# Optimization experiments

Measured on AMD Instinct MI355X. Metric: run time of the kernel, lower is better.

Reference implementation:

```python
import jax, jax.numpy as jnp
import numpy as np

B, S, D, N, R = 4, 2048, 1024, 64, 128

def setup_inputs() -> dict:
    key = jax.random.key(0)
    k1, k2, k3, k4, k5 = jax.random.split(key, 5)
    x = jax.random.normal(k1, (B, S, D), dtype=jnp.float32)
    feature_know_w = jax.random.uniform(k2, (B, S, N), dtype=jnp.float32)
    restore_know_w = jax.random.uniform(k3, (B, S, N), dtype=jnp.float32)
    # neuron pools, scaled like typical init
    feature_know = jax.random.normal(k4, (N, D, R), dtype=jnp.float32) / np.sqrt(D)
    restore_know = jax.random.normal(k5, (N, R, D), dtype=jnp.float32) / np.sqrt(R)
    return {"x": x, "feature_know_w": feature_know_w, "restore_know_w": restore_know_w,
            "feature_know": feature_know, "restore_know": restore_know}

def reference(x, feature_know_w, restore_know_w, feature_know, restore_know):
    # Feature stage: all_h[b,s,n,r] = sum_d x[b,s,d] * feature_know[n,d,r];
    # h[b,s,r] = sum_n all_h[b,s,n,r] * feature_know_w[b,s,n].
    # Fused into one einsum (same math, XLA picks pairwise contraction;
    # largest intermediate is [B,S,N,R], never [B,S,N,D]).
    h = jnp.einsum('bsd,ndr,bsn->bsr', x, feature_know, feature_know_w)
    # Restore stage: all_out[b,s,n,d] = sum_r h[b,s,r] * restore_know[n,r,d];
    # out[b,s,d] = sum_n all_out[b,s,n,d] * restore_know_w[b,s,n].
    # Reordered contraction keeps the intermediate at [B,S,N,R] instead of [B,S,N,D].
    out = jnp.einsum('bsr,bsn,nrd->bsd', h, restore_know_w, restore_know)
    # dropout p=0.0 -> identity
    return out
```

## Files before the change

kernel.cpp:

```cpp
#include <hip/hip_runtime.h>
#include <stdint.h>


typedef unsigned short ushort_t;
typedef __attribute__((ext_vector_type(8))) short frag_t;
typedef __attribute__((ext_vector_type(4))) float f32x4;

#define BK 64

__device__ __forceinline__ unsigned short f2bf(float f) {
    unsigned int u = __builtin_bit_cast(unsigned int, f);
    u = (u + 0x7FFFu + ((u >> 16) & 1u)) >> 16;
    return (unsigned short)u;
}
__device__ __forceinline__ float bf2f_lo(unsigned int v) {
    return __builtin_bit_cast(float, v << 16);
}
__device__ __forceinline__ float bf2f_hi(unsigned int v) {
    return __builtin_bit_cast(float, v & 0xFFFF0000u);
}

__device__ __forceinline__ void glds16(const ushort_t* g, ushort_t* l) {
    __builtin_amdgcn_global_load_lds(
        (const __attribute__((address_space(1))) unsigned int*)g,
        (__attribute__((address_space(3))) unsigned int*)l,
        16, 0, 0);
}

__global__ __launch_bounds__(256) void convert_bf(const float* __restrict__ in,
                                                  ushort_t* __restrict__ out, int n8) {
    int idx = blockIdx.x * 256 + threadIdx.x;
    if (idx >= n8) return;
    const float4 v0 = ((const float4*)in)[idx * 2];
    const float4 v1 = ((const float4*)in)[idx * 2 + 1];
    unsigned short b[8] = { f2bf(v0.x), f2bf(v0.y), f2bf(v0.z), f2bf(v0.w),
                            f2bf(v1.x), f2bf(v1.y), f2bf(v1.z), f2bf(v1.w) };
    ((uint4*)out)[idx] = *(const uint4*)b;
}

__global__ __launch_bounds__(256) void transpose_bf(const float* __restrict__ in,
                                                    ushort_t* __restrict__ out,
                                                    int R, int C,
                                                    long in_bstride, long out_bstride) {
    __shared__ float tile[64][65];
    in  += (long)blockIdx.z * in_bstride;
    out += (long)blockIdx.z * out_bstride;
    const int t  = threadIdx.x;
    const int r0 = blockIdx.x * 64;
    const int c0 = blockIdx.y * 64;
    const int ci = t & 63;
    const int rb = t >> 6;
    #pragma unroll
    for (int p = 0; p < 16; ++p)
        tile[rb + 4 * p][ci] = in[(size_t)(r0 + rb + 4 * p) * C + c0 + ci];
    __syncthreads();
    const int cw = t >> 2;
    const int rg = (t & 3) * 16;
    unsigned short buf[16];
    #pragma unroll
    for (int k = 0; k < 16; ++k)
        buf[k] = f2bf(tile[rg + k][cw]);
    uint4* dst = (uint4*)&out[(size_t)(c0 + cw) * R + r0 + rg];
    dst[0] = *(const uint4*)&buf[0];
    dst[1] = *(const uint4*)&buf[8];
}

__global__ __launch_bounds__(256) void mid_fuse(ushort_t* __restrict__ y,
                                                const float* __restrict__ w1,
                                                const float* __restrict__ w2) {
    const int m    = blockIdx.x * 4 + (threadIdx.x >> 6);
    const int lane = threadIdx.x & 63;
    unsigned int* yrow = (unsigned int*)(y + (size_t)m * 8192);
    const float* w1r = w1 + (size_t)m * 64;
    const float* w2r = w2 + (size_t)m * 64;
    float h0 = 0.f, h1 = 0.f;
    #pragma unroll 16
    for (int n = 0; n < 64; ++n) {
        const unsigned int v = yrow[n * 64 + lane];
        const float w = w1r[n];
        h0 += w * bf2f_lo(v);
        h1 += w * bf2f_hi(v);
    }
    #pragma unroll 16
    for (int n = 0; n < 64; ++n) {
        const float w = w2r[n];
        yrow[n * 64 + lane] =
            (unsigned int)f2bf(w * h0) | ((unsigned int)f2bf(w * h1) << 16);
    }
}

template<bool OUT_BF16>
__global__ __launch_bounds__(256, 3)
void kc_gemm(const ushort_t* __restrict__ Ab, const ushort_t* __restrict__ Bt,
             void* __restrict__ Cout, int ldA, int ldB, int ldC, int ksteps)
{
    __shared__ ushort_t As[128 * BK];
    __shared__ ushort_t Bs[128 * BK];

    const int t    = threadIdx.x;
    const int lane = t & 63;
    const int wv   = t >> 6;
    const int m0   = blockIdx.x * 128;
    const int n0   = blockIdx.y * 128;

    const int wm = (wv & 1) * 64;
    const int wn = (wv >> 1) * 64;
    const int fr = lane & 15;
    const int q  = lane >> 4;
    const int e  = fr & 7;

    int srow[4], scol[4];
    #pragma unroll
    for (int c = 0; c < 4; ++c) {
        const int s = (wv * 4 + c) * 64 + lane;
        srow[c] = s >> 3;
        scol[c] = ((s & 7) ^ (srow[c] & 7)) * 8;
    }

    f32x4 acc[4][4];
    #pragma unroll
    for (int i = 0; i < 4; ++i)
        #pragma unroll
        for (int j = 0; j < 4; ++j)
            acc[i][j] = (f32x4){0.f, 0.f, 0.f, 0.f};

    for (int ss = 0; ss < ksteps; ++ss) {
        const int k0 = ss * BK;

        __syncthreads();
        #pragma unroll
        for (int c = 0; c < 4; ++c)
            glds16(Ab + (size_t)(m0 + srow[c]) * ldA + k0 + scol[c],
                   &As[(wv * 4 + c) * 512]);
        #pragma unroll
        for (int c = 0; c < 4; ++c)
            glds16(Bt + (size_t)(n0 + srow[c]) * ldB + k0 + scol[c],
                   &Bs[(wv * 4 + c) * 512]);
        __syncthreads();

        #pragma unroll
        for (int kk = 0; kk < 2; ++kk) {
            const int csw = (kk * 4 + q) ^ e;
            frag_t a[4], b[4];
            #pragma unroll
            for (int i = 0; i < 4; ++i)
                a[i] = *(const frag_t*)&As[((wm + 16 * i + fr) * 8 + csw) * 8];
            #pragma unroll
            for (int j = 0; j < 4; ++j)
                b[j] = *(const frag_t*)&Bs[((wn + 16 * j + fr) * 8 + csw) * 8];
            #pragma unroll
            for (int i = 0; i < 4; ++i)
                #pragma unroll
                for (int j = 0; j < 4; ++j)
                    acc[i][j] = __builtin_amdgcn_mfma_f32_16x16x32_bf16(
                                    a[i], b[j], acc[i][j], 0, 0, 0);
        }
    }

    #pragma unroll
    for (int i = 0; i < 4; ++i) {
        #pragma unroll
        for (int r = 0; r < 4; ++r) {
            const int gm = m0 + wm + 16 * i + q * 4 + r;
            #pragma unroll
            for (int j = 0; j < 4; ++j) {
                const int gn = n0 + wn + 16 * j + fr;
                if constexpr (OUT_BF16)
                    ((ushort_t*)Cout)[(size_t)gm * ldC + gn] = f2bf(acc[i][j][r]);
                else
                    ((float*)Cout)[(size_t)gm * ldC + gn] = acc[i][j][r];
            }
        }
    }
}

template<int SHIFT, int SEG_STEPS, bool ATOMIC>
__global__ __launch_bounds__(256, 4)
void kc_gemm_fold(const ushort_t* __restrict__ Ab, const float* __restrict__ W,
                  const ushort_t* __restrict__ Bt, float* __restrict__ C,
                  int ldA, int ldB, int ldC, int ksteps)
{
    __shared__ ushort_t As[64 * BK];
    __shared__ ushort_t Bs[128 * BK];
    const int t = threadIdx.x, lane = t & 63, wv = t >> 6;
    const int m0 = blockIdx.x * 64, n0 = blockIdx.y * 128;
    const int kbase = blockIdx.z * ksteps * BK;
    const int wm = (wv & 1) * 32, wn = (wv >> 1) * 64;
    const int fr = lane & 15, q = lane >> 4, e = fr & 7;
    int arow[2], acol[2], brow[4], bcol[4];
    #pragma unroll
    for (int c = 0; c < 2; ++c) {
        const int s = (wv * 2 + c) * 64 + lane;
        arow[c] = s >> 3; acol[c] = ((s & 7) ^ (arow[c] & 7)) * 8;
    }
    #pragma unroll
    for (int c = 0; c < 4; ++c) {
        const int s = (wv * 4 + c) * 64 + lane;
        brow[c] = s >> 3; bcol[c] = ((s & 7) ^ (brow[c] & 7)) * 8;
    }
    f32x4 acc_out[2][4];
    #pragma unroll
    for (int i = 0; i < 2; ++i)
        #pragma unroll
        for (int j = 0; j < 4; ++j) acc_out[i][j] = (f32x4){0.f,0.f,0.f,0.f};
    const int nsegs = ksteps / SEG_STEPS;
    for (int seg = 0; seg < nsegs; ++seg) {
        const int segk = kbase + seg * SEG_STEPS * BK;
        const int nidx = segk >> SHIFT;
        f32x4 acc_in[2][4];
        #pragma unroll
        for (int i = 0; i < 2; ++i)
            #pragma unroll
            for (int j = 0; j < 4; ++j) acc_in[i][j] = (f32x4){0.f,0.f,0.f,0.f};
        for (int ss = 0; ss < SEG_STEPS; ++ss) {
            const int k0 = segk + ss * BK;
            const int d0 = k0 & ((1 << SHIFT) - 1);
            __syncthreads();
            #pragma unroll
            for (int c = 0; c < 2; ++c)
                glds16(Ab + (size_t)(m0 + arow[c]) * ldA + d0 + acol[c],
                       &As[(wv * 2 + c) * 512]);
            #pragma unroll
            for (int c = 0; c < 4; ++c)
                glds16(Bt + (size_t)(n0 + brow[c]) * ldB + k0 + bcol[c],
                       &Bs[(wv * 4 + c) * 512]);
            __syncthreads();
            #pragma unroll
            for (int kk = 0; kk < 2; ++kk) {
                const int csw = (kk * 4 + q) ^ e;
                frag_t a[2], b[4];
                #pragma unroll
                for (int i = 0; i < 2; ++i)
                    a[i] = *(const frag_t*)&As[((wm + 16*i + fr) * 8 + csw) * 8];
                #pragma unroll
                for (int j = 0; j < 4; ++j)
                    b[j] = *(const frag_t*)&Bs[((wn + 16*j + fr) * 8 + csw) * 8];
                #pragma unroll
                for (int i = 0; i < 2; ++i)
                    #pragma unroll
                    for (int j = 0; j < 4; ++j)
                        acc_in[i][j] = __builtin_amdgcn_mfma_f32_16x16x32_bf16(
                                           a[i], b[j], acc_in[i][j], 0, 0, 0);
            }
        }
        #pragma unroll
        for (int i = 0; i < 2; ++i)
            #pragma unroll
            for (int r = 0; r < 4; ++r) {
                const int gm = m0 + wm + 16*i + q*4 + r;
                const float w = W[(size_t)gm * 64 + nidx];
                #pragma unroll
                for (int j = 0; j < 4; ++j) acc_out[i][j][r] += w * acc_in[i][j][r];
            }
    }
    #pragma unroll
    for (int i = 0; i < 2; ++i)
        #pragma unroll
        for (int j = 0; j < 4; ++j)
            #pragma unroll
            for (int r = 0; r < 4; ++r) {
                const int gm = m0 + wm + 16*i + q*4 + r;
                const int gn = n0 + wn + 16*j + fr;
                if constexpr (ATOMIC) atomicAdd(&C[(size_t)gm * ldC + gn], acc_out[i][j][r]);
                else C[(size_t)gm * ldC + gn] = acc_out[i][j][r];
            }
}

extern "C" void kernel_launch(void* const* d_in, const int* in_sizes, int n_in,
                              void* d_out, int out_size, void* d_ws, size_t ws_size,
                              hipStream_t stream) {
    const float* x  = (const float*)d_in[0];
    const float* w1 = (const float*)d_in[1];
    const float* w2 = (const float*)d_in[2];
    const float* F  = (const float*)d_in[3];
    const float* Rk = (const float*)d_in[4];
    float* out = (float*)d_out;

    char* ws = (char*)d_ws;
    const size_t MB = (size_t)1 << 20;

    if (ws_size >= 160 * MB) {
        ushort_t* y    = (ushort_t*)ws;
        ushort_t* x_bf = (ushort_t*)(ws + 128 * MB);
        ushort_t* F_t2 = (ushort_t*)(ws + 144 * MB);
        ushort_t* Rk_t = x_bf;

        convert_bf<<<4096, 256, 0, stream>>>(x, x_bf, 1048576);
        transpose_bf<<<dim3(16, 2, 64), 256, 0, stream>>>(
            F, F_t2, 1024, 128, 131072, 131072);

        kc_gemm<true><<<dim3(64, 64), 256, 0, stream>>>(
            x_bf, F_t2, y, 1024, 1024, 8192, 16);

        mid_fuse<<<2048, 256, 0, stream>>>(y, w1, w2);

        transpose_bf<<<dim3(128, 16, 1), 256, 0, stream>>>(
            Rk, Rk_t, 8192, 1024, 0, 0);

        kc_gemm<false><<<dim3(64, 8), 256, 0, stream>>>(
            y, Rk_t, out, 8192, 8192, 1024, 128);
    } else {
        float*    h    = (float*)ws;
        ushort_t* x_bf = (ushort_t*)(ws + 4  * MB);
        ushort_t* Rk_t = (ushort_t*)(ws + 4  * MB);
        ushort_t* F_t  = (ushort_t*)(ws + 20 * MB);
        ushort_t* h_bf = (ushort_t*)(ws + 36 * MB);

        hipMemsetAsync(h, 0, 4 * MB, stream);
        convert_bf<<<4096, 256, 0, stream>>>(x, x_bf, 1048576);
        transpose_bf<<<dim3(1024, 2, 1), 256, 0, stream>>>(F, F_t, 65536, 128, 0, 0);

        kc_gemm_fold<10, 16, true><<<dim3(128, 1, 8), 256, 0, stream>>>(
            x_bf, w1, F_t, h, 1024, 65536, 128, 128);

        convert_bf<<<512, 256, 0, stream>>>(h, h_bf, 131072);
        transpose_bf<<<dim3(128, 16, 1), 256, 0, stream>>>(Rk, Rk_t, 8192, 1024, 0, 0);

        kc_gemm_fold<7, 2, false><<<dim3(128, 8, 1), 256, 0, stream>>>(
            h_bf, w2, Rk_t, out, 128, 8192, 1024, 128);
    }
}
```

Before: 467.1 us.

## Add 256x256-tile double-buffered GEMM for the feature projection stage

Adds a new GEMM kernel with 256x256 output tiles, 512 threads (8 waves), double-buffered LDS and staged async global-to-LDS loads interleaved with four MFMA phases per k-step. It replaces the 128x128 kernel for the first large GEMM (x times transposed feature pool), with the aim of more data reuse per tile and hiding load latency behind compute. The larger tile needs about 128KB of LDS and many accumulator registers, which limits occupancy and yields only 1024 blocks.

Measured after the change: 516.0 us. 1.1x slower.

```diff
diff --git a/kernel.cpp b/kernel.cpp
--- a/kernel.cpp
+++ b/kernel.cpp
@@ -87,6 +87,135 @@
         yrow[n * 64 + lane] =
             (unsigned int)f2bf(w * h0) | ((unsigned int)f2bf(w * h1) << 16);
     }
+}
+
+template<bool OUT_BF16>
+__global__ __launch_bounds__(512, 2)
+void kc_gemm256(const ushort_t* __restrict__ Ab, const ushort_t* __restrict__ Bt,
+                void* __restrict__ Cout, int ldA, int ldB, int ldC, int ksteps)
+{
+    __shared__ ushort_t As[2][256 * BK];
+    __shared__ ushort_t Bs[2][256 * BK];
+
+    const int t    = threadIdx.x;
+    const int lane = t & 63;
+    const int wv   = t >> 6;
+    const int m0   = blockIdx.x * 256;
+    const int n0   = blockIdx.y * 256;
+
+    const int wm = (wv >> 2) * 128;
+    const int wn = (wv & 3) * 64;
+    const int fr = lane & 15;
+    const int q  = lane >> 4;
+    const int e  = fr & 7;
+    const int lrow = lane >> 3;
+    const int lchk = lane & 7;
+
+    f32x4 acc[8][4];
+    #pragma unroll
+    for (int i = 0; i < 8; ++i)
+        #pragma unroll
+        for (int j = 0; j < 4; ++j)
+            acc[i][j] = (f32x4){0.f, 0.f, 0.f, 0.f};
+
+#define ISSUE_A(abuf, ih, piece, kt) do {                                     \
+        const int r0_ = (piece) * 128 + (ih) * 64 + wv * 8;                   \
+        const int rr_ = r0_ + lrow;                                           \
+        glds16(Ab + (size_t)(m0 + rr_) * ldA + (kt) + ((lchk ^ (rr_ & 7)) << 3), \
+               &As[abuf][r0_ * BK]);                                          \
+    } while (0)
+#define ISSUE_B(bbuf, jh, piece, kt) do {                                     \
+        const int r0_ = (piece) * 128 + (jh) * 32 + wv * 8 + (wv >> 2) * 32;  \
+        const int rr_ = r0_ + lrow;                                           \
+        glds16(Bt + (size_t)(n0 + rr_) * ldB + (kt) + ((lchk ^ (rr_ & 7)) << 3), \
+               &Bs[bbuf][r0_ * BK]);                                          \
+    } while (0)
+#define BAR() do { __builtin_amdgcn_s_barrier();                              \
+                   __builtin_amdgcn_sched_barrier(0); } while (0)
+#define VMCNT(n) do { asm volatile("s_waitcnt vmcnt(" #n ")" ::: "memory");   \
+                      __builtin_amdgcn_sched_barrier(0); } while (0)
+#define PHASE(pbuf, ih, jh) do {                                              \
+        frag_t a_[2][4], b_[2][2];                                            \
+        _Pragma("unroll")                                                     \
+        for (int kk = 0; kk < 2; ++kk) {                                      \
+            const int cs_ = ((kk * 4 + q) ^ e) * 8;                           \
+            _Pragma("unroll")                                                 \
+            for (int ii = 0; ii < 4; ++ii)                                    \
+                a_[kk][ii] = *(const frag_t*)&As[pbuf][                       \
+                    (wm + ((ih) * 4 + ii) * 16 + fr) * BK + cs_];             \
+            _Pragma("unroll")                                                 \
+            for (int jj = 0; jj < 2; ++jj)                                    \
+                b_[kk][jj] = *(const frag_t*)&Bs[pbuf][                       \
+                    (wn + ((jh) * 2 + jj) * 16 + fr) * BK + cs_];             \
+        }                                                                     \
+        __builtin_amdgcn_s_setprio(1);                                        \
+        _Pragma("unroll")                                                     \
+        for (int kk = 0; kk < 2; ++kk)                                        \
+            _Pragma("unroll")                                                 \
+            for (int ii = 0; ii < 4; ++ii)                                    \
+                _Pragma("unroll")                                             \
+                for (int jj = 0; jj < 2; ++jj)                                \
+                    acc[(ih) * 4 + ii][(jh) * 2 + jj] =                       \
+                        __builtin_amdgcn_mfma_f32_16x16x32_bf16(              \
+                            a_[kk][ii], b_[kk][jj],                           \
+                            acc[(ih) * 4 + ii][(jh) * 2 + jj], 0, 0, 0);      \
+        __builtin_amdgcn_s_setprio(0);                                        \
+    } while (0)
+
+    ISSUE_A(0, 0, 0, 0); ISSUE_A(0, 0, 1, 0);
+    ISSUE_A(0, 1, 0, 0); ISSUE_A(0, 1, 1, 0);
+    ISSUE_B(0, 0, 0, 0); ISSUE_B(0, 0, 1, 0);
+    ISSUE_B(0, 1, 0, 0); ISSUE_B(0, 1, 1, 0);
+    if (ksteps > 1) {
+        ISSUE_A(1, 0, 0, BK); ISSUE_A(1, 0, 1, BK);
+        ISSUE_B(1, 0, 0, BK); ISSUE_B(1, 0, 1, BK);
+        VMCNT(4);
+    } else {
+        VMCNT(0);
+    }
+    BAR();
+
+    for (int T = 0; T < ksteps; ++T) {
+        const int buf = T & 1;
+        const int kn1 = (T + 1) * BK;
+        const int kn2 = (T + 2) * BK;
+        if (T + 1 < ksteps) {
+            ISSUE_A(buf ^ 1, 1, 0, kn1); ISSUE_A(buf ^ 1, 1, 1, kn1);
+            ISSUE_B(buf ^ 1, 1, 0, kn1); ISSUE_B(buf ^ 1, 1, 1, kn1);
+        }
+        PHASE(buf, 0, 0);
+        BAR();
+        PHASE(buf, 0, 1);
+        BAR();
+        if (T + 2 < ksteps) { ISSUE_A(buf, 0, 0, kn2); ISSUE_A(buf, 0, 1, kn2); }
+        PHASE(buf, 1, 0);
+        BAR();
+        if (T + 2 < ksteps) { ISSUE_B(buf, 0, 0, kn2); ISSUE_B(buf, 0, 1, kn2); }
+        PHASE(buf, 1, 1);
+        if (T < ksteps - 2) { VMCNT(4); } else { VMCNT(0); }
+        BAR();
+    }
+
+    #pragma unroll
+    for (int i = 0; i < 8; ++i) {
+        #pragma unroll
+        for (int r = 0; r < 4; ++r) {
+            const int gm = m0 + wm + 16 * i + q * 4 + r;
+            #pragma unroll
+            for (int j = 0; j < 4; ++j) {
+                const int gn = n0 + wn + 16 * j + fr;
+                if constexpr (OUT_BF16)
+                    ((ushort_t*)Cout)[(size_t)gm * ldC + gn] = f2bf(acc[i][j][r]);
+                else
+                    ((float*)Cout)[(size_t)gm * ldC + gn] = acc[i][j][r];
+            }
+        }
+    }
+#undef ISSUE_A
+#undef ISSUE_B
+#undef BAR
+#undef VMCNT
+#undef PHASE
 }
 
 template<bool OUT_BF16>
@@ -289,7 +418,7 @@
         transpose_bf<<<dim3(16, 2, 64), 256, 0, stream>>>(
             F, F_t2, 1024, 128, 131072, 131072);
 
-        kc_gemm<true><<<dim3(64, 64), 256, 0, stream>>>(
+        kc_gemm256<true><<<dim3(32, 32), 512, 0, stream>>>(
             x_bf, F_t2, y, 1024, 1024, 8192, 16);
 
         mid_fuse<<<2048, 256, 0, stream>>>(y, w1, w2);
```
